# Kernel tuning notes

Measured on AMD Instinct MI355X. Metric: run time of the kernel, lower is better.

Reference implementation:

```python
import jax, jax.numpy as jnp
import numpy as np

HEADS = 8
MAX_BUCKETS = 128
DIM = 128          # = 2 * d_h
TEMPERATURE = 0.7
SINKHORN_ITERS = 8
EPS = 1e-6


def setup_inputs() -> dict:
    key = jax.random.key(0)
    k1, k2, k3, k4, k5 = jax.random.split(key, 5)
    B, T, DH = 4, 16384, 64
    q = jax.random.normal(k1, (B * HEADS, T, DH), dtype=jnp.float32)
    k = jax.random.normal(k2, (B * HEADS, T, DH), dtype=jnp.float32)
    linear = jax.random.normal(k3, (1, HEADS, DIM, MAX_BUCKETS), dtype=jnp.float32)
    segment_ids = jnp.sort(
        jax.random.randint(k4, (B, T), 0, MAX_BUCKETS), axis=-1
    ).astype(jnp.int32)
    gumbel_u = jax.random.uniform(k5, (B * HEADS, MAX_BUCKETS, MAX_BUCKETS), dtype=jnp.float32)
    return {"q": q, "k": k, "linear": linear, "segment_ids": segment_ids, "gumbel_u": gumbel_u}


def _forward(q, k, linear, segment_ids, gumbel_u):
    bh, t, dh = q.shape           # (b*heads, t, d_h)
    b = segment_ids.shape[0]
    heads = bh // b
    # replicate per-sample bucket assignment across heads (sample-major layout)
    ids = jnp.repeat(segment_ids, heads, axis=0)          # (bh, t)
    seg_sum = jax.vmap(lambda x, s: jax.ops.segment_sum(x, s, num_segments=MAX_BUCKETS))
    sq = seg_sum(q, ids)                                  # (bh, nb, d_h)
    sk = seg_sum(k, ids)                                  # (bh, nb, d_h)
    x = jnp.concatenate([sq, sk], axis=-1)                # (bh, nb, 2*d_h)
    # expand linear over batch and merge head dim: (bh, dim, max_buckets)
    W = jnp.broadcast_to(linear, (b,) + linear.shape[1:]).reshape(bh, DIM, MAX_BUCKETS)
    R = jax.nn.relu(jnp.einsum("bnd,bdm->bnm", x, W))     # (bh, nb, mb)
    # gumbel sinkhorn
    r = jnp.log(R + EPS)
    g = -jnp.log(-jnp.log(gumbel_u + EPS) + EPS)
    r = (r + g) / TEMPERATURE
    for _ in range(SINKHORN_ITERS):
        r = r - jax.nn.logsumexp(r, axis=2, keepdims=True)
        r = r - jax.nn.logsumexp(r, axis=1, keepdims=True)
    return jnp.exp(r)


def reference(q, k, linear, segment_ids, gumbel_u):
    return _forward(q, k, linear, segment_ids, gumbel_u)
```

## Files before the change

### kernel.cpp

```cpp
#include <hip/hip_runtime.h>
#include <hip/hip_bf16.h>

constexpr int HEADS = 8;
constexpr int B = 4;
constexpr int BH = B * HEADS;
constexpr int T = 16384;
constexpr int DH = 64;
constexpr int NB = 128;
constexpr int DIM = 128;
constexpr float EPS = 1e-6f;
constexpr float INV_TEMP = 1.0f / 0.7f;

constexpr int CHUNK = 512;
constexpr int TPG = 64;

__global__ __launch_bounds__(256) void k_segsum(
    const float* __restrict__ q, const float* __restrict__ k,
    const int* __restrict__ seg, float* __restrict__ x) {
  const int bh = blockIdx.y;
  const int b = bh >> 3;
  const int t0 = blockIdx.x * CHUNK;
  const int tid = threadIdx.x;

  __shared__ int ids[CHUNK];
  for (int i = tid; i < CHUNK; i += 256) ids[i] = seg[(size_t)b * T + t0 + i];
  __syncthreads();

  const int slot = tid & 31;
  const int grp = tid >> 5;
  const bool isq = slot < 16;
  const int f4 = slot & 15;
  const int base = grp * TPG;
  const float4* src = (const float4*)((isq ? q : k) + (size_t)bh * T * DH) +
                      (size_t)(t0 + base) * 16 + f4;
  float* xb = x + (size_t)bh * NB * 128 + (isq ? 0 : DH) + f4 * 4;

  float4 acc = make_float4(0.f, 0.f, 0.f, 0.f);
  int cur = ids[base];

  for (int j = 0; j < TPG; j += 8) {
    float4 v[8];
#pragma unroll
    for (int u = 0; u < 8; u++) v[u] = src[(size_t)(j + u) * 16];
#pragma unroll
    for (int u = 0; u < 8; u++) {
      asm volatile("" : "+v"(v[u].x), "+v"(v[u].y), "+v"(v[u].z), "+v"(v[u].w));
    }
    int bk[8];
#pragma unroll
    for (int u = 0; u < 8; u++) bk[u] = ids[base + j + u];

#pragma unroll
    for (int u = 0; u < 8; u++) {
      if (bk[u] != cur) {
        float* p = xb + (size_t)cur * 128;
        atomicAdd(p + 0, acc.x);
        atomicAdd(p + 1, acc.y);
        atomicAdd(p + 2, acc.z);
        atomicAdd(p + 3, acc.w);
        acc = v[u];
        cur = bk[u];
      } else {
        acc.x += v[u].x; acc.y += v[u].y; acc.z += v[u].z; acc.w += v[u].w;
      }
    }
  }
  {
    float* p = xb + (size_t)cur * 128;
    atomicAdd(p + 0, acc.x);
    atomicAdd(p + 1, acc.y);
    atomicAdd(p + 2, acc.z);
    atomicAdd(p + 3, acc.w);
  }
}

__global__ __launch_bounds__(256) void k_matmul(
    const float* __restrict__ x, const float* __restrict__ linear,
    const float* __restrict__ gumbel, float* __restrict__ r0) {
  const int bh = blockIdx.y;
  const int n0 = blockIdx.x * 16;
  const int h = bh & 7;
  const int tid = threadIdx.x;

  __shared__ float xs[16][DIM];

  const float4* xp = (const float4*)(x + ((size_t)bh * NB + n0) * DIM);
  for (int i = tid; i < 16 * 32; i += 256) {
    const float4 v = xp[i];
    const int n = i >> 5, d4 = i & 31;
    xs[n][d4 * 4 + 0] = v.x;
    xs[n][d4 * 4 + 1] = v.y;
    xs[n][d4 * 4 + 2] = v.z;
    xs[n][d4 * 4 + 3] = v.w;
  }
  __syncthreads();

  const int mt = tid & 31;
  const int rp = tid >> 5;
  const int ra = rp * 2;

  float4 a0 = make_float4(0.f, 0.f, 0.f, 0.f);
  float4 a1 = make_float4(0.f, 0.f, 0.f, 0.f);
  const float4* Wp = (const float4*)(linear + (size_t)h * DIM * NB);
  for (int d4 = 0; d4 < 32; d4++) {
    const float4 xv0 = *(const float4*)&xs[ra][d4 * 4];
    const float4 xv1 = *(const float4*)&xs[ra + 1][d4 * 4];
    const float4 w0 = Wp[(d4 * 4 + 0) * 32 + mt];
    const float4 w1 = Wp[(d4 * 4 + 1) * 32 + mt];
    const float4 w2 = Wp[(d4 * 4 + 2) * 32 + mt];
    const float4 w3 = Wp[(d4 * 4 + 3) * 32 + mt];
    a0.x += xv0.x * w0.x + xv0.y * w1.x + xv0.z * w2.x + xv0.w * w3.x;
    a0.y += xv0.x * w0.y + xv0.y * w1.y + xv0.z * w2.y + xv0.w * w3.y;
    a0.z += xv0.x * w0.z + xv0.y * w1.z + xv0.z * w2.z + xv0.w * w3.z;
    a0.w += xv0.x * w0.w + xv0.y * w1.w + xv0.z * w2.w + xv0.w * w3.w;
    a1.x += xv1.x * w0.x + xv1.y * w1.x + xv1.z * w2.x + xv1.w * w3.x;
    a1.y += xv1.x * w0.y + xv1.y * w1.y + xv1.z * w2.y + xv1.w * w3.y;
    a1.z += xv1.x * w0.z + xv1.y * w1.z + xv1.z * w2.z + xv1.w * w3.z;
    a1.w += xv1.x * w0.w + xv1.y * w1.w + xv1.z * w2.w + xv1.w * w3.w;
  }

  const float4* gp = (const float4*)(gumbel + ((size_t)bh * NB + n0) * NB);
  float4* op = (float4*)(r0 + ((size_t)bh * NB + n0) * NB);

  auto xform = [](float a, float u) {
    const float R = fmaxf(a, 0.f);
    const float g = -__logf(-__logf(u + EPS) + EPS);
    return (__logf(R + EPS) + g) * INV_TEMP;
  };
  {
    const float4 u = gp[(size_t)ra * 32 + mt];
    float4 o;
    o.x = xform(a0.x, u.x); o.y = xform(a0.y, u.y);
    o.z = xform(a0.z, u.z); o.w = xform(a0.w, u.w);
    op[(size_t)ra * 32 + mt] = o;
  }
  {
    const float4 u = gp[(size_t)(ra + 1) * 32 + mt];
    float4 o;
    o.x = xform(a1.x, u.x); o.y = xform(a1.y, u.y);
    o.z = xform(a1.z, u.z); o.w = xform(a1.w, u.w);
    op[(size_t)(ra + 1) * 32 + mt] = o;
  }
}

__global__ __launch_bounds__(512) void k_sinkhorn(
    const float* __restrict__ r0, float* __restrict__ out) {
  const int bh = blockIdx.x;
  const int tid = threadIdx.x;

  __shared__ float img[NB * (NB + 1)];
  __shared__ float lse_c[NB];

  const int row = tid >> 2;
  const int qp = tid & 3;

  float rr[32];
  {
    const float4* rp =
        (const float4*)(r0 + (size_t)bh * NB * NB + row * NB + qp * 32);
#pragma unroll
    for (int u = 0; u < 8; u++) {
      const float4 v = rp[u];
      rr[4 * u + 0] = v.x; rr[4 * u + 1] = v.y;
      rr[4 * u + 2] = v.z; rr[4 * u + 3] = v.w;
    }
  }

  for (int it = 0; it < 8; it++) {
    float m = rr[0];
#pragma unroll
    for (int j = 1; j < 32; j++) m = fmaxf(m, rr[j]);
    m = fmaxf(m, __shfl_xor(m, 1));
    m = fmaxf(m, __shfl_xor(m, 2));
    float s = 0.f;
#pragma unroll
    for (int j = 0; j < 32; j++) s += __expf(rr[j] - m);
    s += __shfl_xor(s, 1);
    s += __shfl_xor(s, 2);
    const float lse = m + __logf(s);
#pragma unroll
    for (int j = 0; j < 32; j++) rr[j] -= lse;

#pragma unroll
    for (int j = 0; j < 32; j++) img[row * (NB + 1) + qp * 32 + j] = rr[j];
    __syncthreads();

    float tmp[32];
#pragma unroll
    for (int j = 0; j < 32; j++) {
      const int n = qp * 32 + ((j + qp * 8) & 31);
      tmp[j] = img[n * (NB + 1) + row];
    }
    float cm = tmp[0];
#pragma unroll
    for (int j = 1; j < 32; j++) cm = fmaxf(cm, tmp[j]);
    cm = fmaxf(cm, __shfl_xor(cm, 1));
    cm = fmaxf(cm, __shfl_xor(cm, 2));
    float cs = 0.f;
#pragma unroll
    for (int j = 0; j < 32; j++) cs += __expf(tmp[j] - cm);
    cs += __shfl_xor(cs, 1);
    cs += __shfl_xor(cs, 2);
    if (qp == 0) lse_c[row] = cm + __logf(cs);
    __syncthreads();

#pragma unroll
    for (int j = 0; j < 32; j++) rr[j] -= lse_c[qp * 32 + j];
  }

  {
    float4* op = (float4*)(out + (size_t)bh * NB * NB + row * NB + qp * 32);
#pragma unroll
    for (int u = 0; u < 8; u++) {
      float4 v;
      v.x = __expf(rr[4 * u + 0]);
      v.y = __expf(rr[4 * u + 1]);
      v.z = __expf(rr[4 * u + 2]);
      v.w = __expf(rr[4 * u + 3]);
      op[u] = v;
    }
  }
}

extern "C" void kernel_launch(void* const* d_in, const int* in_sizes, int n_in,
                              void* d_out, int out_size, void* d_ws, size_t ws_size,
                              hipStream_t stream) {
  const float* q = (const float*)d_in[0];
  const float* k = (const float*)d_in[1];
  const float* linear = (const float*)d_in[2];
  const int* seg = (const int*)d_in[3];
  const float* gum = (const float*)d_in[4];
  float* out = (float*)d_out;

  float* x = (float*)d_ws;
  float* r0 = out;

  hipMemsetAsync(x, 0, (size_t)BH * NB * DIM * sizeof(float), stream);

  dim3 g1(T / CHUNK, BH);
  k_segsum<<<g1, 256, 0, stream>>>(q, k, seg, x);

  dim3 g2(8, BH);
  k_matmul<<<g2, 256, 0, stream>>>(x, linear, gum, r0);

  k_sinkhorn<<<BH, 512, 0, stream>>>(r0, out);
}
```

Baseline: 333.0 us.

## Replace atomic segment-sum with sorted bucket boundaries and per-bucket wave reductions

Uses the fact that segment ids are sorted: a small kernel computes the start index of each bucket, then one wavefront per (bh, bucket) sums its contiguous token range directly and writes the result without atomics. This removes the memset and the atomic adds and their contention. In exchange it adds a kernel launch, and buckets are uneven in length, so per-wave work is imbalanced. Each wave also reads only 8-byte float2 per lane instead of float4, so memory access is less vectorised.

```diff
diff --git a/kernel.cpp b/kernel.cpp
--- a/kernel.cpp
+++ b/kernel.cpp
@@ -11,67 +11,64 @@
 constexpr float EPS = 1e-6f;
 constexpr float INV_TEMP = 1.0f / 0.7f;
 
-constexpr int CHUNK = 512;
-constexpr int TPG = 64;
-
-__global__ __launch_bounds__(256) void k_segsum(
+__global__ __launch_bounds__(256) void k_bounds(
+    const int* __restrict__ seg, int* __restrict__ start) {
+  const int b = blockIdx.x;
+  const int tid = threadIdx.x;
+  const int* s = seg + (size_t)b * T;
+  for (int i = tid; i <= T; i += 256) {
+    const int prev = (i == 0) ? -1 : s[i - 1];
+    const int cur = (i == T) ? NB : s[i];
+    for (int v = prev + 1; v <= cur; ++v) start[b * (NB + 1) + v] = i;
+  }
+}
+
+__global__ __launch_bounds__(256) void k_bucketsum(
     const float* __restrict__ q, const float* __restrict__ k,
-    const int* __restrict__ seg, float* __restrict__ x) {
-  const int bh = blockIdx.y;
+    const int* __restrict__ start, float* __restrict__ x) {
+  const int wave = threadIdx.x >> 6;
+  const int lane = threadIdx.x & 63;
+  const int p = blockIdx.x * 4 + wave;
+  const int bh = p >> 7;
+  const int m = p & 127;
   const int b = bh >> 3;
-  const int t0 = blockIdx.x * CHUNK;
-  const int tid = threadIdx.x;
-
-  __shared__ int ids[CHUNK];
-  for (int i = tid; i < CHUNK; i += 256) ids[i] = seg[(size_t)b * T + t0 + i];
-  __syncthreads();
-
-  const int slot = tid & 31;
-  const int grp = tid >> 5;
-  const bool isq = slot < 16;
-  const int f4 = slot & 15;
-  const int base = grp * TPG;
-  const float4* src = (const float4*)((isq ? q : k) + (size_t)bh * T * DH) +
-                      (size_t)(t0 + base) * 16 + f4;
-  float* xb = x + (size_t)bh * NB * 128 + (isq ? 0 : DH) + f4 * 4;
-
-  float4 acc = make_float4(0.f, 0.f, 0.f, 0.f);
-  int cur = ids[base];
-
-  for (int j = 0; j < TPG; j += 8) {
-    float4 v[8];
-#pragma unroll
-    for (int u = 0; u < 8; u++) v[u] = src[(size_t)(j + u) * 16];
-#pragma unroll
-    for (int u = 0; u < 8; u++) {
-      asm volatile("" : "+v"(v[u].x), "+v"(v[u].y), "+v"(v[u].z), "+v"(v[u].w));
-    }
-    int bk[8];
-#pragma unroll
-    for (int u = 0; u < 8; u++) bk[u] = ids[base + j + u];
-
-#pragma unroll
-    for (int u = 0; u < 8; u++) {
-      if (bk[u] != cur) {
-        float* p = xb + (size_t)cur * 128;
-        atomicAdd(p + 0, acc.x);
-        atomicAdd(p + 1, acc.y);
-        atomicAdd(p + 2, acc.z);
-        atomicAdd(p + 3, acc.w);
-        acc = v[u];
-        cur = bk[u];
-      } else {
-        acc.x += v[u].x; acc.y += v[u].y; acc.z += v[u].z; acc.w += v[u].w;
-      }
-    }
-  }
-  {
-    float* p = xb + (size_t)cur * 128;
-    atomicAdd(p + 0, acc.x);
-    atomicAdd(p + 1, acc.y);
-    atomicAdd(p + 2, acc.z);
-    atomicAdd(p + 3, acc.w);
-  }
+
+  const int s = start[b * (NB + 1) + m];
+  const int e = start[b * (NB + 1) + m + 1];
+
+  const int half = lane >> 5;
+  const int li = lane & 31;
+  const float2* src =
+      (const float2*)((half ? k : q) + (size_t)bh * T * DH) + li;
+
+  float2 a = make_float2(0.f, 0.f);
+  int t = s;
+  for (; t + 8 <= e; t += 8) {
+    float2 v0 = src[(size_t)(t + 0) * 32];
+    float2 v1 = src[(size_t)(t + 1) * 32];
+    float2 v2 = src[(size_t)(t + 2) * 32];
+    float2 v3 = src[(size_t)(t + 3) * 32];
+    float2 v4 = src[(size_t)(t + 4) * 32];
+    float2 v5 = src[(size_t)(t + 5) * 32];
+    float2 v6 = src[(size_t)(t + 6) * 32];
+    float2 v7 = src[(size_t)(t + 7) * 32];
+    float2 s01 = make_float2(v0.x + v1.x, v0.y + v1.y);
+    float2 s23 = make_float2(v2.x + v3.x, v2.y + v3.y);
+    float2 s45 = make_float2(v4.x + v5.x, v4.y + v5.y);
+    float2 s67 = make_float2(v6.x + v7.x, v6.y + v7.y);
+    float2 s03 = make_float2(s01.x + s23.x, s01.y + s23.y);
+    float2 s47 = make_float2(s45.x + s67.x, s45.y + s67.y);
+    a.x += s03.x + s47.x;
+    a.y += s03.y + s47.y;
+  }
+  for (; t < e; ++t) {
+    const float2 v = src[(size_t)t * 32];
+    a.x += v.x;
+    a.y += v.y;
+  }
+
+  float2* op = (float2*)(x + ((size_t)bh * NB + m) * DIM + half * DH) + li;
+  *op = a;
 }
 
 __global__ __launch_bounds__(256) void k_matmul(
@@ -233,12 +230,12 @@
   float* out = (float*)d_out;
 
   float* x = (float*)d_ws;
+  int* bounds = (int*)(x + (size_t)BH * NB * DIM);
   float* r0 = out;
 
-  hipMemsetAsync(x, 0, (size_t)BH * NB * DIM * sizeof(float), stream);
-
-  dim3 g1(T / CHUNK, BH);
-  k_segsum<<<g1, 256, 0, stream>>>(q, k, seg, x);
+  k_bounds<<<B, 256, 0, stream>>>(seg, bounds);
+
+  k_bucketsum<<<BH * NB / 4, 256, 0, stream>>>(q, k, bounds, x);
 
   dim3 g2(8, BH);
   k_matmul<<<g2, 256, 0, stream>>>(x, linear, gum, r0);
```

Result: slower. 374.9 us (+12.6%).

## Accumulate bucket sums in shared-memory copies before flushing to global

Applied to the files above, without the earlier changes.

Replaces the segment-sum kernel with a version that uses 1024-token chunks and accumulates per-bucket sums in four padded shared-memory copies via LDS atomics. At the end it flushes them to global with one atomic per element, and falls back to direct global atomics when a chunk covers more than 16 buckets. Loads are issued as inline-asm batches of eight dwordx4 loads with an explicit wait. The aim is to cut global atomic traffic and raise memory-level parallelism, at the cost of an atomic per element in LDS where the old code kept run-length sums in registers.

```diff
diff --git a/kernel.cpp b/kernel.cpp
--- a/kernel.cpp
+++ b/kernel.cpp
@@ -1,5 +1,6 @@
 #include <hip/hip_runtime.h>
 #include <hip/hip_bf16.h>
+#include <stdint.h>
 
 constexpr int HEADS = 8;
 constexpr int B = 4;
@@ -11,66 +12,100 @@
 constexpr float EPS = 1e-6f;
 constexpr float INV_TEMP = 1.0f / 0.7f;
 
-constexpr int CHUNK = 512;
-constexpr int TPG = 64;
-
-__global__ __launch_bounds__(256) void k_segsum(
+constexpr int CHUNK = 1024;
+constexpr int SPAN = 16;
+constexpr int CPAD = SPAN * DIM + 1;
+
+typedef float v4f __attribute__((ext_vector_type(4)));
+
+#define LOAD8(A0, A1, A2, A3)                                               \
+  asm volatile(                                                             \
+      "global_load_dwordx4 %[o0], %[a0], off\n\t"                           \
+      "global_load_dwordx4 %[o1], %[a0], off offset:2048\n\t"               \
+      "global_load_dwordx4 %[o2], %[a1], off\n\t"                           \
+      "global_load_dwordx4 %[o3], %[a1], off offset:2048\n\t"               \
+      "global_load_dwordx4 %[o4], %[a2], off\n\t"                           \
+      "global_load_dwordx4 %[o5], %[a2], off offset:2048\n\t"               \
+      "global_load_dwordx4 %[o6], %[a3], off\n\t"                           \
+      "global_load_dwordx4 %[o7], %[a3], off offset:2048\n\t"               \
+      "s_waitcnt vmcnt(0)"                                                  \
+      : [o0] "=&v"(v0), [o1] "=&v"(v1), [o2] "=&v"(v2), [o3] "=&v"(v3),     \
+        [o4] "=&v"(v4), [o5] "=&v"(v5), [o6] "=&v"(v6), [o7] "=&v"(v7)      \
+      : [a0] "v"(A0), [a1] "v"(A1), [a2] "v"(A2), [a3] "v"(A3)              \
+      : "memory")
+
+__global__ __launch_bounds__(256) void k_bucketsum(
     const float* __restrict__ q, const float* __restrict__ k,
     const int* __restrict__ seg, float* __restrict__ x) {
-  const int bh = blockIdx.y;
+  const int bh = blockIdx.x >> 4;
+  const int c = blockIdx.x & 15;
   const int b = bh >> 3;
-  const int t0 = blockIdx.x * CHUNK;
+  const int t0 = c * CHUNK;
   const int tid = threadIdx.x;
 
   __shared__ int ids[CHUNK];
+  __shared__ float sums[4 * CPAD];
+
   for (int i = tid; i < CHUNK; i += 256) ids[i] = seg[(size_t)b * T + t0 + i];
+  for (int i = tid; i < 4 * CPAD; i += 256) sums[i] = 0.f;
   __syncthreads();
 
-  const int slot = tid & 31;
-  const int grp = tid >> 5;
-  const bool isq = slot < 16;
-  const int f4 = slot & 15;
-  const int base = grp * TPG;
-  const float4* src = (const float4*)((isq ? q : k) + (size_t)bh * T * DH) +
-                      (size_t)(t0 + base) * 16 + f4;
-  float* xb = x + (size_t)bh * NB * 128 + (isq ? 0 : DH) + f4 * 4;
-
-  float4 acc = make_float4(0.f, 0.f, 0.f, 0.f);
-  int cur = ids[base];
-
-  for (int j = 0; j < TPG; j += 8) {
-    float4 v[8];
-#pragma unroll
-    for (int u = 0; u < 8; u++) v[u] = src[(size_t)(j + u) * 16];
-#pragma unroll
-    for (int u = 0; u < 8; u++) {
-      asm volatile("" : "+v"(v[u].x), "+v"(v[u].y), "+v"(v[u].z), "+v"(v[u].w));
-    }
-    int bk[8];
-#pragma unroll
-    for (int u = 0; u < 8; u++) bk[u] = ids[base + j + u];
-
-#pragma unroll
-    for (int u = 0; u < 8; u++) {
-      if (bk[u] != cur) {
-        float* p = xb + (size_t)cur * 128;
-        atomicAdd(p + 0, acc.x);
-        atomicAdd(p + 1, acc.y);
-        atomicAdd(p + 2, acc.z);
-        atomicAdd(p + 3, acc.w);
-        acc = v[u];
-        cur = bk[u];
-      } else {
-        acc.x += v[u].x; acc.y += v[u].y; acc.z += v[u].z; acc.w += v[u].w;
+  const int bmin = ids[0];
+  const int span = ids[CHUNK - 1] - bmin + 1;
+
+  const int w = tid >> 6;
+  const int lane = tid & 63;
+  const int sub = lane >> 4;
+  const int cc = lane & 15;
+  const bool isq = (w < 2);
+  const int slot = (w & 1) * 4 + sub;
+  const float* srcb = (isq ? q : k) + (size_t)bh * T * DH + (size_t)t0 * DH;
+  float* copy = &sums[sub * CPAD];
+  const int coloff = (isq ? 0 : DH) + cc * 4;
+
+  if (span <= SPAN) {
+    const uint64_t base =
+        (uint64_t)(uintptr_t)srcb + (uint64_t)slot * 256 + (uint64_t)cc * 16;
+    for (int i0 = 0; i0 < CHUNK / 8; i0 += 8) {
+      const uint64_t a0 = base + (uint64_t)i0 * 2048;
+      const uint64_t a1 = a0 + 4096;
+      const uint64_t a2 = a0 + 8192;
+      const uint64_t a3 = a0 + 12288;
+      v4f v0, v1, v2, v3, v4, v5, v6, v7;
+      LOAD8(a0, a1, a2, a3);
+      v4f vv[8] = {v0, v1, v2, v3, v4, v5, v6, v7};
+#pragma unroll
+      for (int u = 0; u < 8; u++) {
+        const int row = (i0 + u) * 8 + slot;
+        const int id = ids[row] - bmin;
+        float* d = copy + id * DIM + coloff;
+        atomicAdd(d + 0, vv[u].x);
+        atomicAdd(d + 1, vv[u].y);
+        atomicAdd(d + 2, vv[u].z);
+        atomicAdd(d + 3, vv[u].w);
       }
     }
-  }
-  {
-    float* p = xb + (size_t)cur * 128;
-    atomicAdd(p + 0, acc.x);
-    atomicAdd(p + 1, acc.y);
-    atomicAdd(p + 2, acc.z);
-    atomicAdd(p + 3, acc.w);
+  } else {
+    for (int i = 0; i < CHUNK / 8; i++) {
+      const int row = i * 8 + slot;
+      const float4 v = *(const float4*)(srcb + (size_t)row * DH + cc * 4);
+      float* d = x + ((size_t)bh * NB + ids[row]) * DIM + coloff;
+      atomicAdd(d + 0, v.x);
+      atomicAdd(d + 1, v.y);
+      atomicAdd(d + 2, v.z);
+      atomicAdd(d + 3, v.w);
+    }
+  }
+  __syncthreads();
+
+  if (span <= SPAN) {
+    const int total = span * DIM;
+    float* xp = x + ((size_t)bh * NB + bmin) * DIM;
+    for (int i = tid; i < total; i += 256) {
+      const float vsum = sums[0 * CPAD + i] + sums[1 * CPAD + i] +
+                         sums[2 * CPAD + i] + sums[3 * CPAD + i];
+      atomicAdd(&xp[i], vsum);
+    }
   }
 }
 
@@ -237,8 +272,7 @@
 
   hipMemsetAsync(x, 0, (size_t)BH * NB * DIM * sizeof(float), stream);
 
-  dim3 g1(T / CHUNK, BH);
-  k_segsum<<<g1, 256, 0, stream>>>(q, k, seg, x);
+  k_bucketsum<<<BH * (T / CHUNK), 256, 0, stream>>>(q, k, seg, x);
 
   dim3 g2(8, BH);
   k_matmul<<<g2, 256, 0, stream>>>(x, linear, gum, r0);
```

New measurement: 569.7 us. 71.1% more time.
